# Performance work log

Measured on AMD Instinct MI355X. Metric: run time of the kernel, lower is better.

Reference implementation:

```python
import jax, jax.numpy as jnp
import numpy as np

V, E, H, L, HID, T, B = 50257, 512, 8, 8, 1365, 1024, 2
HD = E // H
EPS = 1e-5


def setup_inputs() -> dict:
    key = jax.random.key(0)
    ks = jax.random.split(key, 9)
    s = 0.02
    def nrm(k, shape):
        return jax.random.normal(k, shape, jnp.float32) * s
    return {
        "idx": jax.random.randint(ks[0], (B, T), 0, V),
        "W_emb": nrm(ks[1], (V, E)),          # tied tok_emb / lm head
        "pos_emb": nrm(ks[2], (T, E)),
        "ln1_s": jnp.ones((L, E)), "ln1_b": jnp.zeros((L, E)),
        "qkv_w": nrm(ks[3], (L, E, 3 * E)),
        "proj_w": nrm(ks[4], (L, E, E)),
        "ln2_s": jnp.ones((L, E)), "ln2_b": jnp.zeros((L, E)),
        "gate_w": nrm(ks[5], (L, E, HID)),
        "up_w": nrm(ks[6], (L, E, HID)),
        "down_w": nrm(ks[7], (L, HID, E)),
        "lnf_s": jnp.ones((E,)), "lnf_b": jnp.zeros((E,)),
    }


def _ln(x, s, b):
    m = x.mean(-1, keepdims=True)
    v = ((x - m) ** 2).mean(-1, keepdims=True)
    return (x - m) * jax.lax.rsqrt(v + EPS) * s + b


def _forward(idx, W_emb, pos_emb, ln1_s, ln1_b, qkv_w, proj_w,
             ln2_s, ln2_b, gate_w, up_w, down_w, lnf_s, lnf_b):
    x = W_emb[idx] + pos_emb[None, :, :]  # [B,T,E]
    pos = jnp.arange(T)
    # faithful to source: ALiBi bias uses |i-j|, added before causal mask
    dist = jnp.abs(pos[None, :] - pos[:, None]).astype(jnp.float32)  # [T,T]
    slopes = (1.0 / 2.0 ** (8.0 * jnp.arange(1, H + 1, dtype=jnp.float32) / H))
    alibi = slopes[:, None, None] * dist[None]  # [H,T,T]
    causal = jnp.tril(jnp.ones((T, T), bool))
    scale = 1.0 / np.sqrt(HD)

    def block(x, p):
        l1s, l1b, qkvw, pw, l2s, l2b, gw, uw, dw = p
        h = _ln(x, l1s, l1b)
        qkv = h @ qkvw  # [B,T,3E]
        q, k, v = jnp.split(qkv, 3, axis=-1)
        q = q.reshape(B, T, H, HD).transpose(0, 2, 1, 3)
        k = k.reshape(B, T, H, HD).transpose(0, 2, 1, 3)
        v = v.reshape(B, T, H, HD).transpose(0, 2, 1, 3)
        att = jnp.einsum('bhqd,bhkd->bhqk', q, k) * scale + alibi[None]
        att = jnp.where(causal, att, -jnp.inf)
        att = jax.nn.softmax(att, axis=-1)
        o = jnp.einsum('bhqk,bhkd->bhqd', att, v)
        o = o.transpose(0, 2, 1, 3).reshape(B, T, E)
        x = x + o @ pw
        h = _ln(x, l2s, l2b)
        g = h @ gw
        x = x + (g * jax.nn.sigmoid(g) * (h @ uw)) @ dw  # SwiGLU
        return x, None

    x, _ = jax.lax.scan(block, x, (ln1_s, ln1_b, qkv_w, proj_w,
                                   ln2_s, ln2_b, gate_w, up_w, down_w))
    x = _ln(x, lnf_s, lnf_b)
    return x @ W_emb.T  # tied head -> [B,T,V]


def reference(idx, W_emb, pos_emb, ln1_s, ln1_b, qkv_w, proj_w,
              ln2_s, ln2_b, gate_w, up_w, down_w, lnf_s, lnf_b):
    return _forward(idx, W_emb, pos_emb, ln1_s, ln1_b, qkv_w, proj_w,
                    ln2_s, ln2_b, gate_w, up_w, down_w, lnf_s, lnf_b)
```

## Files before the change

kernel.cpp:

```cpp
#include <hip/hip_runtime.h>
#include <hip/hip_bf16.h>
#include <math.h>

#define V_SZ 50257
#define V_PAD 50304
#define E_SZ 512
#define H_N 8
#define L_N 8
#define HID_SZ 1365
#define HID_PAD 1408
#define T_SZ 1024
#define B_SZ 2
#define HD_SZ 64
#define ROWS (B_SZ * T_SZ)

typedef short bf16x8 __attribute__((ext_vector_type(8)));
typedef float f32x4 __attribute__((ext_vector_type(4)));
typedef float f32x16 __attribute__((ext_vector_type(16)));

__global__ __launch_bounds__(128) void embed_kernel(
    const int* __restrict__ idx, const float* __restrict__ W,
    const float* __restrict__ P, float* __restrict__ x,
    float* __restrict__ stats) {
  const int bt = blockIdx.x;
  const int t = bt & (T_SZ - 1);
  const int id = idx[bt];
  const int e = threadIdx.x * 4;
  float4 w = *(const float4*)(W + (size_t)id * E_SZ + e);
  float4 p = *(const float4*)(P + (size_t)t * E_SZ + e);
  float4 r;
  r.x = w.x + p.x; r.y = w.y + p.y; r.z = w.z + p.z; r.w = w.w + p.w;
  *(float4*)(x + (size_t)bt * E_SZ + e) = r;
  float s = r.x + r.y + r.z + r.w;
  float q = r.x * r.x + r.y * r.y + r.z * r.z + r.w * r.w;
#pragma unroll
  for (int o = 32; o; o >>= 1) { s += __shfl_xor(s, o); q += __shfl_xor(q, o); }
  __shared__ float sr[4];
  if ((threadIdx.x & 63) == 0) {
    sr[(threadIdx.x >> 6) * 2] = s;
    sr[(threadIdx.x >> 6) * 2 + 1] = q;
  }
  __syncthreads();
  if (threadIdx.x < 16) {
    float a = (threadIdx.x == 0) ? sr[0] + sr[2] : 0.f;
    float b2 = (threadIdx.x == 0) ? sr[1] + sr[3] : 0.f;
    float* st = stats + (size_t)bt * 32 + threadIdx.x * 2;
    st[0] = a; st[1] = b2;
  }
}

__global__ __launch_bounds__(256) void ln_from_stats(
    const float* __restrict__ x, const float* __restrict__ stats,
    const float* __restrict__ gamma, const float* __restrict__ beta,
    __hip_bfloat16* __restrict__ out) {
  const int row = blockIdx.x;
  const int tid = threadIdx.x;
  const float* sp = stats + (size_t)row * 32;
  float sum = 0.f, ssq = 0.f;
#pragma unroll
  for (int i = 0; i < 8; ++i) {
    float4 v = ((const float4*)sp)[i];
    sum += v.x + v.z; ssq += v.y + v.w;
  }
  const float mean = sum * (1.f / 512.f);
  const float var = ssq * (1.f / 512.f) - mean * mean;
  const float rstd = rsqrtf(var + 1e-5f);
  const float2 v = *(const float2*)(x + (size_t)row * E_SZ + tid * 2);
  const float2 sv = *(const float2*)(gamma + tid * 2);
  const float2 bv = *(const float2*)(beta + tid * 2);
  __hip_bfloat162 ov;
  ov.x = __float2bfloat16((v.x - mean) * rstd * sv.x + bv.x);
  ov.y = __float2bfloat16((v.y - mean) * rstd * sv.y + bv.y);
  *(__hip_bfloat162*)(out + (size_t)row * E_SZ + tid * 2) = ov;
}

__global__ __launch_bounds__(256) void convert_wemb(
    const float* __restrict__ W, __hip_bfloat16* __restrict__ Wb) {
  const int tid = blockIdx.x * 256 + threadIdx.x;
  const int row = tid >> 6;
  const int c = (tid & 63) * 8;
  union { __hip_bfloat16 h[8]; int4 v; } u;
  if (row < V_SZ) {
    const float* p = W + (size_t)row * E_SZ + c;
#pragma unroll
    for (int j = 0; j < 8; ++j) u.h[j] = __float2bfloat16(p[j]);
  } else {
#pragma unroll
    for (int j = 0; j < 8; ++j) u.h[j] = __float2bfloat16(0.f);
  }
  *(int4*)(Wb + (size_t)row * E_SZ + c) = u.v;
}

__global__ __launch_bounds__(256) void transp_convert(
    const float* __restrict__ in, __hip_bfloat16* __restrict__ out,
    int K, int N, int Kpad, int Npad) {
  __shared__ float tile[32][33];
  const int l = blockIdx.z;
  in  += (size_t)l * K * N;
  out += (size_t)l * Npad * Kpad;
  const int tx = threadIdx.x & 31, ty = threadIdx.x >> 5;
  const int n0 = blockIdx.x * 32, k0 = blockIdx.y * 32;
#pragma unroll
  for (int i = 0; i < 4; ++i) {
    const int k = k0 + ty + i * 8, n = n0 + tx;
    tile[ty + i * 8][tx] = (k < K && n < N) ? in[(size_t)k * N + n] : 0.f;
  }
  __syncthreads();
#pragma unroll
  for (int i = 0; i < 4; ++i) {
    const int n = n0 + ty + i * 8, kk = k0 + tx;
    out[(size_t)n * Kpad + kk] = __float2bfloat16(tile[tx][ty + i * 8]);
  }
}

__global__ __launch_bounds__(256) void gu_prep(
    const float* __restrict__ gate, const float* __restrict__ up,
    __hip_bfloat16* __restrict__ outw) {
  __shared__ float tile[32][33];
  const int l = blockIdx.z;
  const int c0 = blockIdx.x * 32, k0 = blockIdx.y * 32;
  const int tx = threadIdx.x & 31, ty = threadIdx.x >> 5;
#pragma unroll
  for (int role = 0; role < 2; ++role) {
    const float* src = (role ? up : gate) + (size_t)l * E_SZ * HID_SZ;
#pragma unroll
    for (int i = 0; i < 4; ++i) {
      const int k = k0 + ty + i * 8, c = c0 + tx;
      tile[ty + i * 8][tx] = (c < HID_SZ) ? src[(size_t)k * HID_SZ + c] : 0.f;
    }
    __syncthreads();
#pragma unroll
    for (int i = 0; i < 4; ++i) {
      const int c = c0 + ty + i * 8, kk = k0 + tx;
      const int n = ((c >> 4) << 5) | (role << 4) | (c & 15);
      outw[((size_t)l * 2816 + n) * E_SZ + kk] = __float2bfloat16(tile[tx][ty + i * 8]);
    }
    __syncthreads();
  }
}

template <int EPI>
__global__ __launch_bounds__(256) void gemm64ln(
    const float* __restrict__ X, const __hip_bfloat16* __restrict__ B,
    void* __restrict__ Cv, const float* __restrict__ stats,
    const float* __restrict__ gamma, const float* __restrict__ beta,
    int N, int K) {
  __shared__ char lds[16384];
  __shared__ float gb[1024];
  const int tid = threadIdx.x, lane = tid & 63, w = tid >> 6;
  const int wr = w >> 1, wc = w & 1;
  const int m0 = blockIdx.y * 64, n0 = blockIdx.x * 64;
  const size_t SB = (size_t)K * 2;
  char* As = lds;
  char* Bs = lds + 8192;
  const char* Bb = (const char*)B + (size_t)n0 * SB;
  f32x4 acc[2][2] = {};
  const int lrow = lane >> 3;
  const int schunk = ((lane & 7) ^ lrow) * 16;
  const int kb = (lane >> 4) * 16;

  for (int i = tid; i < 512; i += 256) { gb[i] = gamma[i]; gb[512 + i] = beta[i]; }

  const int arow = tid >> 2, acol = (tid & 3) * 16;
  const int achunk0 = acol >> 3;
  const int akey = arow & 7;
  float mean, rstd;
  {
    const float* sp = stats + (size_t)(m0 + arow) * 32;
    float sum = 0.f, ssq = 0.f;
#pragma unroll
    for (int i = 0; i < 8; ++i) {
      float4 v = ((const float4*)sp)[i];
      sum += v.x + v.z; ssq += v.y + v.w;
    }
    mean = sum * (1.f / 512.f);
    const float var = ssq * (1.f / 512.f) - mean * mean;
    rstd = rsqrtf(var + 1e-5f);
  }
  const float* Xrow = X + (size_t)(m0 + arow) * K;
  __syncthreads();

  for (int k0 = 0; k0 < K; k0 += 64) {
#pragma unroll
    for (int i = 0; i < 2; ++i) {
      const int row = w * 8 + 32 * i + lrow;
      const char* gbp = Bb + (size_t)row * SB + k0 * 2 + schunk;
      __builtin_amdgcn_global_load_lds(
          (const __attribute__((address_space(1))) unsigned int*)gbp,
          (__attribute__((address_space(3))) unsigned int*)(Bs + w * 1024 + i * 4096),
          16, 0, 0);
    }
    {
      float xf[16];
      const float* xs = Xrow + k0 + acol;
      *(float4*)&xf[0]  = ((const float4*)xs)[0];
      *(float4*)&xf[4]  = ((const float4*)xs)[1];
      *(float4*)&xf[8]  = ((const float4*)xs)[2];
      *(float4*)&xf[12] = ((const float4*)xs)[3];
      union { __hip_bfloat16 h[16]; int4 v[2]; } pk;
#pragma unroll
      for (int jj = 0; jj < 16; ++jj) {
        const int col = k0 + acol + jj;
        pk.h[jj] = __float2bfloat16((xf[jj] - mean) * rstd * gb[col] + gb[512 + col]);
      }
      *(int4*)(As + arow * 128 + (((achunk0 + 0) ^ akey) * 16)) = pk.v[0];
      *(int4*)(As + arow * 128 + (((achunk0 + 1) ^ akey) * 16)) = pk.v[1];
    }
    __syncthreads();
    bf16x8 a[2][2], bb[2][2];
#pragma unroll
    for (int i = 0; i < 2; ++i) {
      const int ra = wr * 32 + i * 16 + (lane & 15);
      const int rb = wc * 32 + i * 16 + (lane & 15);
#pragma unroll
      for (int ks = 0; ks < 2; ++ks) {
        a[i][ks]  = *(const bf16x8*)(As + ra * 128 + ((ks * 64 + kb) ^ ((ra & 7) << 4)));
        bb[i][ks] = *(const bf16x8*)(Bs + rb * 128 + ((ks * 64 + kb) ^ ((rb & 7) << 4)));
      }
    }
#pragma unroll
    for (int ks = 0; ks < 2; ++ks)
#pragma unroll
      for (int i = 0; i < 2; ++i)
#pragma unroll
        for (int j = 0; j < 2; ++j)
          acc[i][j] = __builtin_amdgcn_mfma_f32_16x16x32_bf16(a[i][ks], bb[j][ks], acc[i][j], 0, 0, 0);
    __syncthreads();
  }

  const int cr = (lane >> 4) * 4, ccol = lane & 15;
  if (EPI == 3) {
    __hip_bfloat16* G = (__hip_bfloat16*)Cv;
    const int cg = (n0 >> 1) + wc * 16 + ccol;
#pragma unroll
    for (int i = 0; i < 2; ++i) {
#pragma unroll
      for (int rr = 0; rr < 4; ++rr) {
        const int m = m0 + wr * 32 + i * 16 + cr + rr;
        const float gv = acc[i][0][rr];
        const float uv = acc[i][1][rr];
        const float val = gv / (1.f + __expf(-gv)) * uv;
        G[(size_t)m * HID_PAD + cg] = __float2bfloat16(val);
      }
    }
  } else {
    __hip_bfloat16* O = (__hip_bfloat16*)Cv;
#pragma unroll
    for (int i = 0; i < 2; ++i)
#pragma unroll
      for (int j = 0; j < 2; ++j) {
        const int n = n0 + wc * 32 + j * 16 + ccol;
#pragma unroll
        for (int rr = 0; rr < 4; ++rr) {
          const int m = m0 + wr * 32 + i * 16 + cr + rr;
          O[(size_t)m * N + n] = __float2bfloat16(acc[i][j][rr]);
        }
      }
  }
}

__global__ __launch_bounds__(256) void gemm64(
    const __hip_bfloat16* __restrict__ A, const __hip_bfloat16* __restrict__ B,
    float* __restrict__ C, const float* __restrict__ R,
    float* __restrict__ stats, int N, int K) {
  __shared__ char lds[16384];
  const int tid = threadIdx.x, lane = tid & 63, w = tid >> 6;
  const int wr = w >> 1, wc = w & 1;
  const int m0 = blockIdx.y * 64, n0 = blockIdx.x * 64;
  const size_t SA = (size_t)K * 2;
  char* As = lds;
  char* Bs = lds + 8192;
  const char* Ab = (const char*)A + (size_t)m0 * SA;
  const char* Bb = (const char*)B + (size_t)n0 * SA;
  f32x4 acc[2][2] = {};
  const int lrow = lane >> 3;
  const int schunk = ((lane & 7) ^ lrow) * 16;
  const int kb = (lane >> 4) * 16;

  for (int k0 = 0; k0 < K; k0 += 64) {
#pragma unroll
    for (int i = 0; i < 2; ++i) {
      const int row = w * 8 + 32 * i + lrow;
      const char* ga = Ab + (size_t)row * SA + k0 * 2 + schunk;
      __builtin_amdgcn_global_load_lds(
          (const __attribute__((address_space(1))) unsigned int*)ga,
          (__attribute__((address_space(3))) unsigned int*)(As + w * 1024 + i * 4096),
          16, 0, 0);
      const char* gbp = Bb + (size_t)row * SA + k0 * 2 + schunk;
      __builtin_amdgcn_global_load_lds(
          (const __attribute__((address_space(1))) unsigned int*)gbp,
          (__attribute__((address_space(3))) unsigned int*)(Bs + w * 1024 + i * 4096),
          16, 0, 0);
    }
    __syncthreads();
    bf16x8 a[2][2], bb[2][2];
#pragma unroll
    for (int i = 0; i < 2; ++i) {
      const int ra = wr * 32 + i * 16 + (lane & 15);
      const int rb = wc * 32 + i * 16 + (lane & 15);
#pragma unroll
      for (int ks = 0; ks < 2; ++ks) {
        a[i][ks]  = *(const bf16x8*)(As + ra * 128 + ((ks * 64 + kb) ^ ((ra & 7) << 4)));
        bb[i][ks] = *(const bf16x8*)(Bs + rb * 128 + ((ks * 64 + kb) ^ ((rb & 7) << 4)));
      }
    }
#pragma unroll
    for (int ks = 0; ks < 2; ++ks)
#pragma unroll
      for (int i = 0; i < 2; ++i)
#pragma unroll
        for (int j = 0; j < 2; ++j)
          acc[i][j] = __builtin_amdgcn_mfma_f32_16x16x32_bf16(a[i][ks], bb[j][ks], acc[i][j], 0, 0, 0);
    __syncthreads();
  }

  const int cr = (lane >> 4) * 4, ccol = lane & 15;
  float vv[2][2][4];
#pragma unroll
  for (int i = 0; i < 2; ++i)
#pragma unroll
    for (int j = 0; j < 2; ++j) {
      const int n = n0 + wc * 32 + j * 16 + ccol;
#pragma unroll
      for (int rr = 0; rr < 4; ++rr) {
        const int m = m0 + wr * 32 + i * 16 + cr + rr;
        const float v = acc[i][j][rr] + R[(size_t)m * N + n];
        vv[i][j][rr] = v;
        C[(size_t)m * N + n] = v;
      }
    }
  const int slice = blockIdx.x * 2 + wc;
#pragma unroll
  for (int i = 0; i < 2; ++i) {
#pragma unroll
    for (int rr = 0; rr < 4; ++rr) {
      float s = vv[i][0][rr] + vv[i][1][rr];
      float q = vv[i][0][rr] * vv[i][0][rr] + vv[i][1][rr] * vv[i][1][rr];
#pragma unroll
      for (int o = 1; o < 16; o <<= 1) { s += __shfl_xor(s, o); q += __shfl_xor(q, o); }
      if ((lane & 15) == 0) {
        const int m = m0 + wr * 32 + i * 16 + cr + rr;
        float* st = stats + (size_t)m * 32 + slice * 2;
        st[0] = s; st[1] = q;
      }
    }
  }
}

__global__ __launch_bounds__(256) void head_gemm(
    const __hip_bfloat16* __restrict__ A, const __hip_bfloat16* __restrict__ B,
    float* __restrict__ C, int N, int K) {
  __shared__ char lds[65536];
  const int tid = threadIdx.x;
  const int lane = tid & 63, w = tid >> 6;
  const int wr = w >> 1, wc = w & 1;
  const int nwg = gridDim.x * gridDim.y;
  const int id = blockIdx.y * gridDim.x + blockIdx.x;
  const int work = (id & 7) * (nwg >> 3) + (id >> 3);
  const int bx = work >> 4, by = work & 15;
  const int m0 = by * 128, n0 = bx * 128;
  const size_t SA = (size_t)K * 2;

  f32x4 acc[4][4] = {};
  const char* Ab = (const char*)A + (size_t)m0 * SA;
  const char* Bb = (const char*)B + (size_t)n0 * SA;

  const int lrow = lane >> 3;
  const int schunk = ((lane & 7) ^ lrow) * 16;
  const int kb = (lane >> 4) * 16;

  auto STAGE = [&](int buf, int k0) {
    char* As = lds + buf * 32768;
    char* Bs = As + 16384;
#pragma unroll
    for (int i = 0; i < 4; ++i) {
      const int row = w * 8 + 32 * i + lrow;
      const char* ga = Ab + (size_t)row * SA + k0 * 2 + schunk;
      __builtin_amdgcn_global_load_lds(
          (const __attribute__((address_space(1))) unsigned int*)ga,
          (__attribute__((address_space(3))) unsigned int*)(As + w * 1024 + i * 4096),
          16, 0, 0);
      const char* gbp = Bb + (size_t)row * SA + k0 * 2 + schunk;
      __builtin_amdgcn_global_load_lds(
          (const __attribute__((address_space(1))) unsigned int*)gbp,
          (__attribute__((address_space(3))) unsigned int*)(Bs + w * 1024 + i * 4096),
          16, 0, 0);
    }
  };

  const int NT = 8;
  STAGE(0, 0);
  __syncthreads();
  for (int t = 0; t < NT; ++t) {
    const int cur = t & 1;
    if (t + 1 < NT) STAGE(cur ^ 1, (t + 1) * 64);
    const char* As = lds + cur * 32768;
    const char* Bs = As + 16384;
    bf16x8 a[4][2], b[4][2];
#pragma unroll
    for (int i = 0; i < 4; ++i) {
      const int ra = wr * 64 + i * 16 + (lane & 15);
      const int rb = wc * 64 + i * 16 + (lane & 15);
#pragma unroll
      for (int ks = 0; ks < 2; ++ks) {
        a[i][ks] = *(const bf16x8*)(As + ra * 128 + ((ks * 64 + kb) ^ ((ra & 7) << 4)));
        b[i][ks] = *(const bf16x8*)(Bs + rb * 128 + ((ks * 64 + kb) ^ ((rb & 7) << 4)));
      }
    }
    __builtin_amdgcn_s_setprio(1);
#pragma unroll
    for (int ks = 0; ks < 2; ++ks)
#pragma unroll
      for (int i = 0; i < 4; ++i)
#pragma unroll
        for (int j = 0; j < 4; ++j)
          acc[i][j] = __builtin_amdgcn_mfma_f32_16x16x32_bf16(a[i][ks], b[j][ks], acc[i][j], 0, 0, 0);
    __builtin_amdgcn_s_setprio(0);
    __syncthreads();
  }

  const int cr = (lane >> 4) * 4, ccol = lane & 15;
#pragma unroll
  for (int i = 0; i < 4; ++i) {
#pragma unroll
    for (int j = 0; j < 4; ++j) {
      const int n = n0 + wc * 64 + j * 16 + ccol;
      if (n >= N) continue;
#pragma unroll
      for (int rr = 0; rr < 4; ++rr) {
        const int m = m0 + wr * 64 + i * 16 + cr + rr;
        C[(size_t)m * N + n] = acc[i][j][rr];
      }
    }
  }
}

__global__ __launch_bounds__(256, 1) void attn_mfma_kernel(
    const __hip_bfloat16* __restrict__ qkv, __hip_bfloat16* __restrict__ o) {
  const int bid = blockIdx.x;
  const int qb = bid & 15;
  const int h = (bid >> 4) & 7;
  const int b = bid >> 7;
  const int tid = threadIdx.x;
  const int w = tid >> 6, lane = tid & 63;
  const int g = w >> 1;
  const int wq = w & 1;
  const int l31 = lane & 31, hi = lane >> 5;
  const int q0w = qb * 64 + 32 * wq;
  const float slope = exp2f(-(float)(h + 1));
  const int rowstride = 3 * E_SZ;
  const int nch = (qb + 2) >> 1;
  const int niter = (nch + 1) >> 1;

  __shared__ char lds[65536];
  char* Kb = lds + g * 32768;
  char* Vb = Kb + 16384;

  bf16x8 qf[4];
  {
    const __hip_bfloat16* qrow = qkv + (size_t)(b * T_SZ + q0w + l31) * rowstride + h * HD_SZ;
#pragma unroll
    for (int dblk = 0; dblk < 4; ++dblk)
      qf[dblk] = *(const bf16x8*)(qrow + dblk * 16 + hi * 8);
  }

  f32x16 oacc[2][2] = {};
  float m[2] = {-INFINITY, -INFINITY}, lsum[2] = {0.f, 0.f};

  int4 kreg[8];
  int4 vr[4][2];
  const int ltid = tid & 127;
  const int jK = ltid;
  const int jqV = ltid >> 2, qtV = ltid & 3;
  const int d0V = qtV * 16;

  auto ISSUE = [&](int c) {
    const __hip_bfloat16* srcK = qkv + (size_t)(b * T_SZ + c * 128 + jK) * rowstride + E_SZ + h * HD_SZ;
#pragma unroll
    for (int ch = 0; ch < 8; ++ch) kreg[ch] = ((const int4*)srcK)[ch];
    const __hip_bfloat16* srcV = qkv + (size_t)(b * T_SZ + c * 128 + jqV * 4) * rowstride + 2 * E_SZ + h * HD_SZ + d0V;
#pragma unroll
    for (int rr = 0; rr < 4; ++rr) {
      vr[rr][0] = ((const int4*)(srcV + rr * rowstride))[0];
      vr[rr][1] = ((const int4*)(srcV + rr * rowstride))[1];
    }
  };
  auto WRITE = [&]() {
#pragma unroll
    for (int ch = 0; ch < 8; ++ch)
      *(int4*)(Kb + jK * 128 + ((ch * 16) ^ ((jK & 7) << 4))) = kreg[ch];
    union { int4 v[2]; unsigned short us[16]; } r0, r1, r2, r3;
    r0.v[0] = vr[0][0]; r0.v[1] = vr[0][1];
    r1.v[0] = vr[1][0]; r1.v[1] = vr[1][1];
    r2.v[0] = vr[2][0]; r2.v[1] = vr[2][1];
    r3.v[0] = vr[3][0]; r3.v[1] = vr[3][1];
#pragma unroll
    for (int e = 0; e < 16; ++e) {
      const int d = d0V + e;
      uint2 wv;
      wv.x = (unsigned)r0.us[e] | ((unsigned)r1.us[e] << 16);
      wv.y = (unsigned)r2.us[e] | ((unsigned)r3.us[e] << 16);
      *(uint2*)(Vb + d * 256 + ((jqV * 8) ^ ((d & 7) << 4))) = wv;
    }
  };

  if (g < nch) ISSUE(g);
  for (int i = 0; i < niter; ++i) {
    const int c = 2 * i + g;
    const bool act = c < nch;
    if (act) WRITE();
    __syncthreads();
    if (c + 2 < nch) ISSUE(c + 2);
    if (act) {
      const char* Kl = Kb;
      const char* Vl = Vb;
#pragma unroll
      for (int s = 0; s < 4; ++s) {
        const int j0 = c * 128 + 32 * s;
        if (j0 <= q0w + 31) {
          const int st = s & 1;
          f32x16 sacc = {};
          const int jrow = 32 * s + l31;
          __builtin_amdgcn_s_setprio(1);
#pragma unroll
          for (int dblk = 0; dblk < 4; ++dblk) {
            bf16x8 kf = *(const bf16x8*)(Kl + jrow * 128 + ((dblk * 32 + hi * 16) ^ ((jrow & 7) << 4)));
            sacc = __builtin_amdgcn_mfma_f32_32x32x16_bf16(kf, qf[dblk], sacc, 0, 0, 0);
          }
          __builtin_amdgcn_s_setprio(0);
          const int qg = q0w + l31;
          float p[16];
          float tmax = -1e30f;
#pragma unroll
          for (int r = 0; r < 16; ++r) {
            const int jg = j0 + (r & 3) + 8 * (r >> 2) + 4 * hi;
            const float sv = (jg > qg) ? -1e9f : (sacc[r] * 0.125f + slope * (float)(qg - jg));
            p[r] = sv;
            tmax = fmaxf(tmax, sv);
          }
          tmax = fmaxf(tmax, __shfl_xor(tmax, 32));
          if (!__all(tmax <= m[st] + 8.f)) {
            const float mnew = fmaxf(m[st], tmax);
            const float corr = __expf(m[st] - mnew);
            lsum[st] *= corr;
#pragma unroll
            for (int dt = 0; dt < 2; ++dt)
#pragma unroll
              for (int r = 0; r < 16; ++r) oacc[st][dt][r] *= corr;
            m[st] = mnew;
          }
          float tsum = 0.f;
#pragma unroll
          for (int r = 0; r < 16; ++r) {
            p[r] = __expf(p[r] - m[st]);
            tsum += p[r];
          }
          tsum += __shfl_xor(tsum, 32);
          lsum[st] += tsum;
          unsigned wds[8];
#pragma unroll
          for (int k = 0; k < 8; ++k) {
            union { __hip_bfloat16 hh[2]; unsigned u; } pk_;
            pk_.hh[0] = __float2bfloat16(p[2 * k]);
            pk_.hh[1] = __float2bfloat16(p[2 * k + 1]);
            wds[k] = pk_.u;
          }
          bf16x8 pfrag[2];
#pragma unroll
          for (int jb = 0; jb < 2; ++jb) {
            const unsigned w0 = wds[4 * jb + 0], w1 = wds[4 * jb + 1];
            const unsigned w2 = wds[4 * jb + 2], w3 = wds[4 * jb + 3];
            const unsigned x2 = (unsigned)__shfl_xor((int)w2, 32);
            const unsigned x3 = (unsigned)__shfl_xor((int)w3, 32);
            const unsigned x0 = (unsigned)__shfl_xor((int)w0, 32);
            const unsigned x1 = (unsigned)__shfl_xor((int)w1, 32);
            union { unsigned u[4]; bf16x8 v; } pf;
            pf.u[0] = hi ? x2 : w0;
            pf.u[1] = hi ? x3 : w1;
            pf.u[2] = hi ? w2 : x0;
            pf.u[3] = hi ? w3 : x1;
            pfrag[jb] = pf.v;
          }
          __builtin_amdgcn_s_setprio(1);
#pragma unroll
          for (int dt = 0; dt < 2; ++dt) {
            const int row = dt * 32 + l31;
#pragma unroll
            for (int jb = 0; jb < 2; ++jb) {
              bf16x8 vt = *(const bf16x8*)(Vl + row * 256 + ((s * 64 + jb * 32 + hi * 16) ^ ((row & 7) << 4)));
              oacc[st][dt] = __builtin_amdgcn_mfma_f32_32x32x16_bf16(vt, pfrag[jb], oacc[st][dt], 0, 0, 0);
            }
          }
          __builtin_amdgcn_s_setprio(0);
        }
      }
    }
    __syncthreads();
  }

  float mW, lW;
  float Ow[2][16];
  if (g < nch) {
    const float mm = fmaxf(m[0], m[1]);
    const float a = __expf(m[0] - mm), b2 = __expf(m[1] - mm);
    mW = mm;
    lW = lsum[0] * a + lsum[1] * b2;
#pragma unroll
    for (int dt = 0; dt < 2; ++dt)
#pragma unroll
      for (int r = 0; r < 16; ++r)
        Ow[dt][r] = oacc[0][dt][r] * a + oacc[1][dt][r] * b2;
  } else {
    mW = -INFINITY; lW = 0.f;
#pragma unroll
    for (int dt = 0; dt < 2; ++dt)
#pragma unroll
      for (int r = 0; r < 16; ++r) Ow[dt][r] = 0.f;
  }

  float* Obuf = (float*)lds + wq * 2048;
  float* mlb  = (float*)lds + 4096 + wq * 64;
  __syncthreads();
  if (g == 1) {
#pragma unroll
    for (int dt = 0; dt < 2; ++dt)
#pragma unroll
      for (int r = 0; r < 16; ++r)
        Obuf[lane * 32 + dt * 16 + r] = Ow[dt][r];
    if (hi == 0) { mlb[l31 * 2] = mW; mlb[l31 * 2 + 1] = lW; }
  }
  __syncthreads();
  if (g == 0) {
    const float m1 = mlb[l31 * 2], l1 = mlb[l31 * 2 + 1];
    const float mmF = fmaxf(mW, m1);
    const float wA = __expf(mW - mmF), wB = __expf(m1 - mmF);
    const float inv = 1.f / (lW * wA + l1 * wB);
    __hip_bfloat16* orow = o + (size_t)(b * T_SZ + q0w + l31) * E_SZ + h * HD_SZ;
#pragma unroll
    for (int dt = 0; dt < 2; ++dt) {
#pragma unroll
      for (int gq = 0; gq < 4; ++gq) {
        union { __hip_bfloat16 hh[4]; short4 v; } ov;
#pragma unroll
        for (int e = 0; e < 4; ++e) {
          const int r = 4 * gq + e;
          const float o1 = Obuf[lane * 32 + dt * 16 + r];
          ov.hh[e] = __float2bfloat16((Ow[dt][r] * wA + o1 * wB) * inv);
        }
        *(short4*)(orow + dt * 32 + 4 * hi + 8 * gq) = ov.v;
      }
    }
  }
}

extern "C" void kernel_launch(void* const* d_in, const int* in_sizes, int n_in,
                              void* d_out, int out_size, void* d_ws, size_t ws_size,
                              hipStream_t stream) {
  const int* idx      = (const int*)d_in[0];
  const float* W_emb  = (const float*)d_in[1];
  const float* pos    = (const float*)d_in[2];
  const float* ln1_s  = (const float*)d_in[3];
  const float* ln1_b  = (const float*)d_in[4];
  const float* qkv_w  = (const float*)d_in[5];
  const float* proj_w = (const float*)d_in[6];
  const float* ln2_s  = (const float*)d_in[7];
  const float* ln2_b  = (const float*)d_in[8];
  const float* gate_w = (const float*)d_in[9];
  const float* up_w   = (const float*)d_in[10];
  const float* down_w = (const float*)d_in[11];
  const float* lnf_s  = (const float*)d_in[12];
  const float* lnf_b  = (const float*)d_in[13];
  float* out = (float*)d_out;

  char* p = (char*)d_ws;
  auto alloc = [&](size_t bytes) { char* q = p; p += (bytes + 255) & ~255ULL; return q; };
  float* x      = (float*)alloc((size_t)ROWS * E_SZ * 4);
  float* statsA = (float*)alloc((size_t)ROWS * 32 * 4);
  float* statsB = (float*)alloc((size_t)ROWS * 32 * 4);
  __hip_bfloat16* qkv_bf = (__hip_bfloat16*)alloc((size_t)ROWS * 3 * E_SZ * 2);
  __hip_bfloat16* h_bf  = (__hip_bfloat16*)alloc((size_t)ROWS * E_SZ * 2);
  __hip_bfloat16* o_bf  = (__hip_bfloat16*)alloc((size_t)ROWS * E_SZ * 2);
  __hip_bfloat16* g_bf  = (__hip_bfloat16*)alloc((size_t)ROWS * HID_PAD * 2);
  __hip_bfloat16* Wb    = (__hip_bfloat16*)alloc((size_t)V_PAD * E_SZ * 2);
  __hip_bfloat16* qkvwb = (__hip_bfloat16*)alloc((size_t)L_N * 3 * E_SZ * E_SZ * 2);
  __hip_bfloat16* projwb= (__hip_bfloat16*)alloc((size_t)L_N * E_SZ * E_SZ * 2);
  __hip_bfloat16* guwb  = (__hip_bfloat16*)alloc((size_t)L_N * 2816 * E_SZ * 2);
  __hip_bfloat16* downwb= (__hip_bfloat16*)alloc((size_t)L_N * E_SZ * HID_PAD * 2);

  convert_wemb<<<(V_PAD * E_SZ / 8 + 255) / 256, 256, 0, stream>>>(W_emb, Wb);
  transp_convert<<<dim3(3 * E_SZ / 32, E_SZ / 32, L_N), 256, 0, stream>>>(
      qkv_w, qkvwb, E_SZ, 3 * E_SZ, E_SZ, 3 * E_SZ);
  transp_convert<<<dim3(E_SZ / 32, E_SZ / 32, L_N), 256, 0, stream>>>(
      proj_w, projwb, E_SZ, E_SZ, E_SZ, E_SZ);
  gu_prep<<<dim3(HID_PAD / 32, E_SZ / 32, L_N), 256, 0, stream>>>(gate_w, up_w, guwb);
  transp_convert<<<dim3(E_SZ / 32, HID_PAD / 32, L_N), 256, 0, stream>>>(
      down_w, downwb, HID_SZ, E_SZ, HID_PAD, E_SZ);

  embed_kernel<<<ROWS, 128, 0, stream>>>(idx, W_emb, pos, x, statsA);

  for (int l = 0; l < L_N; ++l) {
    gemm64ln<1><<<dim3(3 * E_SZ / 64, ROWS / 64), 256, 0, stream>>>(
        x, qkvwb + (size_t)l * 3 * E_SZ * E_SZ, qkv_bf, statsA,
        ln1_s + l * E_SZ, ln1_b + l * E_SZ, 3 * E_SZ, E_SZ);
    attn_mfma_kernel<<<B_SZ * H_N * (T_SZ / 64), 256, 0, stream>>>(qkv_bf, o_bf);
    gemm64<<<dim3(E_SZ / 64, ROWS / 64), 256, 0, stream>>>(
        o_bf, projwb + (size_t)l * E_SZ * E_SZ, x, x, statsB, E_SZ, E_SZ);
    gemm64ln<3><<<dim3(2816 / 64, ROWS / 64), 256, 0, stream>>>(
        x, guwb + (size_t)l * 2816 * E_SZ, g_bf, statsB,
        ln2_s + l * E_SZ, ln2_b + l * E_SZ, 2816, E_SZ);
    gemm64<<<dim3(E_SZ / 64, ROWS / 64), 256, 0, stream>>>(
        g_bf, downwb + (size_t)l * E_SZ * HID_PAD, x, x, statsA, E_SZ, HID_PAD);
  }

  ln_from_stats<<<ROWS, 256, 0, stream>>>(x, statsA, lnf_s, lnf_b, h_bf);
  head_gemm<<<dim3(V_PAD / 128, 16), 256, 0, stream>>>(h_bf, Wb, out, V_SZ, E_SZ);
}
```

Measured before the change: 1.224 ms.

## Triple-buffer head GEMM LDS staging with finer K tiles and manual vmcnt waits

Restructures the LM-head GEMM mainloop from double-buffered 64-element K tiles to triple-buffered 32-element K tiles. Loads are issued two stages ahead, and waits use explicit s_waitcnt vmcnt counts plus raw barriers instead of __syncthreads. It also reduces LDS use from 64KB to 48KB and changes the swizzle to match 64-byte rows. The aim is to keep more loads in flight and overlap global-to-LDS traffic with MFMA work. The cost is twice as many barrier pairs per K step and fragile hand-counted waits.

```diff
diff --git a/kernel.cpp b/kernel.cpp
--- a/kernel.cpp
+++ b/kernel.cpp
@@ -350,7 +350,7 @@
 __global__ __launch_bounds__(256) void head_gemm(
     const __hip_bfloat16* __restrict__ A, const __hip_bfloat16* __restrict__ B,
     float* __restrict__ C, int N, int K) {
-  __shared__ char lds[65536];
+  __shared__ char lds[49152];
   const int tid = threadIdx.x;
   const int lane = tid & 63, w = tid >> 6;
   const int wr = w >> 1, wc = w & 1;
@@ -365,58 +365,60 @@
   const char* Ab = (const char*)A + (size_t)m0 * SA;
   const char* Bb = (const char*)B + (size_t)n0 * SA;
 
-  const int lrow = lane >> 3;
-  const int schunk = ((lane & 7) ^ lrow) * 16;
-  const int kb = (lane >> 4) * 16;
-
-  auto STAGE = [&](int buf, int k0) {
-    char* As = lds + buf * 32768;
-    char* Bs = As + 16384;
-#pragma unroll
-    for (int i = 0; i < 4; ++i) {
-      const int row = w * 8 + 32 * i + lrow;
-      const char* ga = Ab + (size_t)row * SA + k0 * 2 + schunk;
+  const int srow = tid >> 2, schnk = tid & 3;
+
+  auto STAGE = [&](int buf, int t) {
+    char* As = lds + buf * 16384;
+    char* Bs = As + 8192;
+    const int k0b = t * 64;
+#pragma unroll
+    for (int i = 0; i < 2; ++i) {
+      const int r = srow + i * 64;
+      const int gc = (schnk ^ (r & 3)) * 16;
+      const char* ga = Ab + (size_t)r * SA + k0b + gc;
       __builtin_amdgcn_global_load_lds(
           (const __attribute__((address_space(1))) unsigned int*)ga,
-          (__attribute__((address_space(3))) unsigned int*)(As + w * 1024 + i * 4096),
+          (__attribute__((address_space(3))) unsigned int*)(As + i * 4096 + tid * 16),
           16, 0, 0);
-      const char* gbp = Bb + (size_t)row * SA + k0 * 2 + schunk;
+      const char* gbp = Bb + (size_t)r * SA + k0b + gc;
       __builtin_amdgcn_global_load_lds(
           (const __attribute__((address_space(1))) unsigned int*)gbp,
-          (__attribute__((address_space(3))) unsigned int*)(Bs + w * 1024 + i * 4096),
+          (__attribute__((address_space(3))) unsigned int*)(Bs + i * 4096 + tid * 16),
           16, 0, 0);
     }
   };
 
-  const int NT = 8;
+  const int kb = lane >> 4;
   STAGE(0, 0);
-  __syncthreads();
-  for (int t = 0; t < NT; ++t) {
-    const int cur = t & 1;
-    if (t + 1 < NT) STAGE(cur ^ 1, (t + 1) * 64);
-    const char* As = lds + cur * 32768;
-    const char* Bs = As + 16384;
-    bf16x8 a[4][2], b[4][2];
+  STAGE(1, 1);
+#pragma unroll
+  for (int t = 0; t < 16; ++t) {
+    if (t + 2 < 16) STAGE((t + 2) % 3, t + 2);
+    if (t <= 13)      asm volatile("s_waitcnt vmcnt(8)" ::: "memory");
+    else if (t == 14) asm volatile("s_waitcnt vmcnt(4)" ::: "memory");
+    else              asm volatile("s_waitcnt vmcnt(0)" ::: "memory");
+    __builtin_amdgcn_s_barrier();
+    asm volatile("" ::: "memory");
+    const char* As = lds + (t % 3) * 16384;
+    const char* Bs = As + 8192;
+    bf16x8 a[4], b[4];
 #pragma unroll
     for (int i = 0; i < 4; ++i) {
       const int ra = wr * 64 + i * 16 + (lane & 15);
       const int rb = wc * 64 + i * 16 + (lane & 15);
-#pragma unroll
-      for (int ks = 0; ks < 2; ++ks) {
-        a[i][ks] = *(const bf16x8*)(As + ra * 128 + ((ks * 64 + kb) ^ ((ra & 7) << 4)));
-        b[i][ks] = *(const bf16x8*)(Bs + rb * 128 + ((ks * 64 + kb) ^ ((rb & 7) << 4)));
-      }
+      a[i] = *(const bf16x8*)(As + ra * 64 + ((kb ^ (ra & 3)) * 16));
+      b[i] = *(const bf16x8*)(Bs + rb * 64 + ((kb ^ (rb & 3)) * 16));
     }
     __builtin_amdgcn_s_setprio(1);
 #pragma unroll
-    for (int ks = 0; ks < 2; ++ks)
-#pragma unroll
-      for (int i = 0; i < 4; ++i)
-#pragma unroll
-        for (int j = 0; j < 4; ++j)
-          acc[i][j] = __builtin_amdgcn_mfma_f32_16x16x32_bf16(a[i][ks], b[j][ks], acc[i][j], 0, 0, 0);
+    for (int i = 0; i < 4; ++i)
+#pragma unroll
+      for (int j = 0; j < 4; ++j)
+        acc[i][j] = __builtin_amdgcn_mfma_f32_16x16x32_bf16(a[i], b[j], acc[i][j], 0, 0, 0);
     __builtin_amdgcn_s_setprio(0);
-    __syncthreads();
+    asm volatile("" ::: "memory");
+    __builtin_amdgcn_s_barrier();
+    asm volatile("" ::: "memory");
   }
 
   const int cr = (lane >> 4) * 4, ccol = lane & 15;
```

Result: faster. 1.199 ms (-2.1%).
